# Optimization experiments

Measured on AMD Instinct MI355X. Metric: run time of the kernel, lower is better.

## Reference

```python
import jax, jax.numpy as jnp
import numpy as np

N_HEADS = 16


def _rope(x, cos, sin):
    # x: (B,H,S,hd); cos,sin: (1,1,S,hd//2). Full-dim rotation (rot_dim == head_dim).
    xe = x[..., 0::2]
    xo = x[..., 1::2]
    re = xe * cos - xo * sin
    ro = xe * sin + xo * cos
    return jnp.stack([re, ro], axis=-1).reshape(x.shape)


def setup_inputs() -> dict:
    key = jax.random.key(0)
    B, S, D = 2, 2048, 1024
    hd = D // N_HEADS
    k1, k2, k3, k4, k5 = jax.random.split(key, 5)
    x = jax.random.normal(k1, (B, S, D), dtype=jnp.float32)
    # Linear params (lecun-normal-ish scale)
    w_qkv = jax.random.normal(k2, (D, 3 * D), dtype=jnp.float32) / np.sqrt(D)
    b_qkv = jnp.zeros((3 * D,), dtype=jnp.float32)
    w_out = jax.random.normal(k3, (D, D), dtype=jnp.float32) / np.sqrt(D)
    b_out = jnp.zeros((D,), dtype=jnp.float32)
    # Rotary tables: (S, hd//2)
    inv_freq = 1.0 / (10000.0 ** (np.arange(0, hd, 2, dtype=np.float32) / hd))
    angles = jnp.asarray(np.arange(S, dtype=np.float32)[:, None] * inv_freq[None, :])
    cos = jnp.cos(angles)
    sin = jnp.sin(angles)
    # Causal mask (seq, seq), True = attend
    mask = jnp.tril(jnp.ones((S, S), dtype=bool))
    return {"x": x, "w_qkv": w_qkv, "b_qkv": b_qkv, "w_out": w_out,
            "b_out": b_out, "cos": cos, "sin": sin, "mask": mask}


def reference(x, w_qkv, b_qkv, w_out, b_out, cos, sin, mask):
    B, S, D = x.shape
    H = N_HEADS
    hd = D // H
    scale = hd ** (-0.5)
    qkv = x @ w_qkv + b_qkv  # (B,S,3D)
    qkv = qkv.reshape(B, S, 3, H, hd).transpose(2, 0, 3, 1, 4)  # (3,B,H,S,hd)
    q, k, v = qkv[0], qkv[1], qkv[2]
    c = cos[None, None, :, :]
    s = sin[None, None, :, :]
    q = _rope(q, c, s)
    k = _rope(k, c, s)
    attn = jnp.einsum('bhqd,bhkd->bhqk', q, k) * scale
    attn = jnp.where(mask, attn, -1e9)
    attn = jax.nn.softmax(attn, axis=-1)
    out = jnp.einsum('bhqk,bhkd->bhqd', attn, v)
    out = out.transpose(0, 2, 1, 3).reshape(B, S, D)
    return out @ w_out + b_out
```

## Files before the change

### kernel.cpp

```cpp
#include <hip/hip_runtime.h>
#include <stdint.h>

typedef unsigned short u16;
typedef __attribute__((ext_vector_type(8))) __bf16 bf16x8;
typedef __attribute__((ext_vector_type(4))) float f32x4;
typedef __attribute__((ext_vector_type(4))) unsigned short u16x4;

__device__ __forceinline__ float bf2f(u16 u){
  unsigned int x = ((unsigned int)u) << 16;
  return __builtin_bit_cast(float, x);
}
__device__ __forceinline__ u16 f2bf(float f){
  return __builtin_bit_cast(u16, (__bf16)f);
}
__device__ __forceinline__ float fexp2(float x){ return __builtin_exp2f(x); }
__device__ __forceinline__ void lds_load16(const void* g, void* l){
  __builtin_amdgcn_global_load_lds(
      (const __attribute__((address_space(1))) unsigned int*)g,
      (__attribute__((address_space(3))) unsigned int*)l, 16, 0, 0);
}

__global__ __launch_bounds__(256) void transpose64(const float* __restrict__ in,
                                                   u16* __restrict__ out,
                                                   int R, int C){
  __shared__ u16 t[64][65];
  const int c0 = blockIdx.x * 64, r0 = blockIdx.y * 64;
  const int tid = threadIdx.x;
  const int rr = tid >> 3;
  const int cc = (tid & 7) * 8;
#pragma unroll
  for (int i = 0; i < 2; i++){
    int r = i * 32 + rr;
    const float* p = in + (size_t)(r0 + r) * C + c0 + cc;
    f32x4 v0 = *(const f32x4*)p;
    f32x4 v1 = *(const f32x4*)(p + 4);
#pragma unroll
    for (int j = 0; j < 4; j++){ t[r][cc + j] = f2bf(v0[j]); t[r][cc + 4 + j] = f2bf(v1[j]); }
  }
  __syncthreads();
#pragma unroll
  for (int i = 0; i < 2; i++){
    int c = i * 32 + rr;
    u16 tmp[8];
#pragma unroll
    for (int j = 0; j < 8; j++) tmp[j] = t[cc + j][c];
    *(bf16x8*)(out + (size_t)(c0 + c) * R + r0 + cc) = *(const bf16x8*)tmp;
  }
}

__global__ __launch_bounds__(256) void convert_bf16(const float* __restrict__ in,
                                                    u16* __restrict__ out){
  int t = blockIdx.x * 256 + threadIdx.x;
  const float* p = in + (size_t)t * 8;
  f32x4 v0 = *(const f32x4*)p;
  f32x4 v1 = *(const f32x4*)(p + 4);
  u16 tmp[8];
#pragma unroll
  for (int j = 0; j < 4; j++){ tmp[j] = f2bf(v0[j]); tmp[4 + j] = f2bf(v1[j]); }
  *(bf16x8*)(out + (size_t)t * 8) = *(const bf16x8*)tmp;
}

__global__ __launch_bounds__(256) void v_transpose(const u16* __restrict__ qkv,
                                                   u16* __restrict__ vT){
  const int S = 2048, LD = 3072;
  __shared__ u16 t[64][65];
  const int bh = blockIdx.y;
  const int b = bh >> 4, h = bh & 15;
  const int s0 = blockIdx.x * 64;
  const u16* src = qkv + (size_t)b * S * LD + 2048 + h * 64;
  const int tid = threadIdx.x;
  const int rr = tid >> 3;
  const int cc = (tid & 7) * 8;
#pragma unroll
  for (int i = 0; i < 2; i++){
    int s = i * 32 + rr;
    bf16x8 v = *(const bf16x8*)(src + (size_t)(s0 + s) * LD + cc);
#pragma unroll
    for (int j = 0; j < 8; j++) t[s][cc + j] = __builtin_bit_cast(u16, (__bf16)v[j]);
  }
  __syncthreads();
  u16* dst = vT + (size_t)bh * 64 * S;
#pragma unroll
  for (int i = 0; i < 2; i++){
    int d = i * 32 + rr;
    u16 tmp[8];
#pragma unroll
    for (int j = 0; j < 8; j++) tmp[j] = t[cc + j][d];
    *(bf16x8*)(dst + (size_t)d * S + s0 + cc) = *(const bf16x8*)tmp;
  }
}

template<bool OUTF32, bool ROPE>
__global__ __launch_bounds__(256, 2) void gemm_bt(const u16* __restrict__ A,
                                                  const u16* __restrict__ Bt,
                                                  const float* __restrict__ bias,
                                                  void* __restrict__ Cv,
                                                  int M, int N, int K,
                                                  const float* __restrict__ cosb,
                                                  const float* __restrict__ sinb){
  __shared__ u16 As[128 * 32];
  __shared__ u16 Bs[128 * 32];
  const int nx = gridDim.x;
  const int L = blockIdx.x + nx * blockIdx.y;
  const int per = (nx * gridDim.y) >> 3;
  const int wg = (L & 7) * per + (L >> 3);
  const int bn = wg % nx, bm = wg / nx;
  const int tid = threadIdx.x, w = tid >> 6, l = tid & 63;
  const int lo = l & 15, hi = l >> 4;
  const int wr = (w >> 1) * 64, wc = (w & 1) * 64;
  f32x4 acc[4][4] = {};
  const int lrow = l >> 2, lcd = l & 3;

  for (int k0 = 0; k0 < K; k0 += 32){
#pragma unroll
    for (int i = 0; i < 2; i++){
      int row0 = i * 64 + w * 16;
      int row = row0 + lrow;
      int cs = lcd ^ ((row >> 1) & 3);
      lds_load16(A  + (size_t)(bm * 128 + row) * K + k0 + cs * 8,
                 (char*)As + row0 * 64);
      lds_load16(Bt + (size_t)(bn * 128 + row) * K + k0 + cs * 8,
                 (char*)Bs + row0 * 64);
    }
    __syncthreads();
    bf16x8 a[4], b[4];
#pragma unroll
    for (int mi = 0; mi < 4; mi++){
      int row = wr + mi * 16 + lo;
      unsigned byte = (unsigned)(row * 64 + hi * 16) ^ (((row >> 1) & 3) << 4);
      a[mi] = *(const bf16x8*)((const char*)As + byte);
    }
#pragma unroll
    for (int ni = 0; ni < 4; ni++){
      int row = wc + ni * 16 + lo;
      unsigned byte = (unsigned)(row * 64 + hi * 16) ^ (((row >> 1) & 3) << 4);
      b[ni] = *(const bf16x8*)((const char*)Bs + byte);
    }
    __builtin_amdgcn_s_setprio(1);
#pragma unroll
    for (int mi = 0; mi < 4; mi++)
#pragma unroll
      for (int ni = 0; ni < 4; ni++)
        acc[mi][ni] = __builtin_amdgcn_mfma_f32_16x16x32_bf16(a[mi], b[ni], acc[mi][ni], 0, 0, 0);
    __builtin_amdgcn_s_setprio(0);
    __syncthreads();
  }
  if (ROPE && bn < 16){
#pragma unroll
    for (int mi = 0; mi < 4; mi++){
#pragma unroll
      for (int r = 0; r < 4; r++){
        int grow = bm * 128 + wr + mi * 16 + hi * 4 + r;
        int stok = grow & 2047;
#pragma unroll
        for (int ni = 0; ni < 4; ni++){
          int col = bn * 128 + wc + ni * 16 + lo;
          float v = acc[mi][ni][r] + bias[col];
          float partner = __shfl_xor(v, 1, 64);
          int ip = (col & 63) >> 1;
          float c = cosb[stok * 32 + ip], sn = sinb[stok * 32 + ip];
          float res = (lo & 1) ? (partner * sn + v * c) : (v * c - partner * sn);
          ((u16*)Cv)[(size_t)grow * N + col] = f2bf(res);
        }
      }
    }
  } else {
#pragma unroll
    for (int mi = 0; mi < 4; mi++){
#pragma unroll
      for (int r = 0; r < 4; r++){
        int grow = bm * 128 + wr + mi * 16 + hi * 4 + r;
#pragma unroll
        for (int ni = 0; ni < 4; ni++){
          int col = bn * 128 + wc + ni * 16 + lo;
          float v = acc[mi][ni][r] + bias[col];
          if (OUTF32)
            ((float*)Cv)[(size_t)grow * N + col] = v;
          else
            ((u16*)Cv)[(size_t)grow * N + col] = f2bf(v);
        }
      }
    }
  }
}

__global__ __launch_bounds__(64, 4) void flash_attn(const u16* __restrict__ qkv,
                                                    const u16* __restrict__ vT,
                                                    u16* __restrict__ Oout){
  const int S = 2048, LD = 3072;
  const int L = blockIdx.x;
  const int bh = L & 31;
  const int p = 63 - (L >> 5);
  const int b = bh >> 4, h = bh & 15;
  const u16* base = qkv + (size_t)b * S * LD;
  const u16* Qp = base + h * 64;
  const u16* Kp = base + 1024 + h * 64;
  const u16* Vb = vT + (size_t)bh * 64 * S;
  const int l = threadIdx.x & 63;
  const int lo = l & 15, hi = l >> 4;
  __shared__ u16 Ks[2][32 * 64];
  __shared__ u16 PsA[16 * 36];
  __shared__ u16 PsB[16 * 36];

  const float QSC = 0.125f * 1.44269504089f;
  const int srow8 = l >> 3;
  const int scs = (l & 7) ^ srow8;

  const int q0 = p * 32;
  const int qrowA = q0 + lo;
  const int qrowB = q0 + 16 + lo;
  const int nkt = p + 1;

  bf16x8 qfA0, qfA1, qfB0, qfB1;
  {
    bf16x8 va0 = *(const bf16x8*)(Qp + (size_t)qrowA * LD + hi * 8);
    bf16x8 va1 = *(const bf16x8*)(Qp + (size_t)qrowA * LD + 32 + hi * 8);
    bf16x8 vb0 = *(const bf16x8*)(Qp + (size_t)qrowB * LD + hi * 8);
    bf16x8 vb1 = *(const bf16x8*)(Qp + (size_t)qrowB * LD + 32 + hi * 8);
#pragma unroll
    for (int j = 0; j < 8; j++){
      qfA0[j] = (__bf16)((float)va0[j] * QSC);
      qfA1[j] = (__bf16)((float)va1[j] * QSC);
      qfB0[j] = (__bf16)((float)vb0[j] * QSC);
      qfB1[j] = (__bf16)((float)vb1[j] * QSC);
    }
  }

  f32x4 oA[4] = {}, oB[4] = {};
  float m_rA = -1e30f, l_parA = 0.f;
  float m_rB = -1e30f, l_parB = 0.f;

#pragma unroll
  for (int i = 0; i < 4; i++)
    lds_load16(Kp + (size_t)(i * 8 + srow8) * LD + scs * 8,
               (char*)&Ks[0][0] + i * 1024);

  int cur = 0;
  for (int kt = 0; kt < nkt; kt++){
    bf16x8 vb[4];
#pragma unroll
    for (int fd = 0; fd < 4; fd++)
      vb[fd] = *(const bf16x8*)(Vb + (size_t)(fd * 16 + lo) * S + kt * 32 + hi * 8);
    bf16x8 kb[2][2];
#pragma unroll
    for (int c = 0; c < 2; c++)
#pragma unroll
      for (int f = 0; f < 2; f++){
        int srow = f * 16 + lo;
        unsigned byte = ((unsigned)(srow * 128 + c * 64 + hi * 16)) ^ ((lo & 7) << 4);
        kb[c][f] = *(const bf16x8*)((const char*)&Ks[cur][0] + byte);
      }
    if (kt + 1 < nkt){
#pragma unroll
      for (int i = 0; i < 4; i++)
        lds_load16(Kp + (size_t)((kt + 1) * 32 + i * 8 + srow8) * LD + scs * 8,
                   (char*)&Ks[cur ^ 1][0] + i * 1024);
    }
    f32x4 saA[2] = {}, saB[2] = {};
    __builtin_amdgcn_s_setprio(1);
#pragma unroll
    for (int f = 0; f < 2; f++){
      saA[f] = __builtin_amdgcn_mfma_f32_16x16x32_bf16(kb[0][f], qfA0, saA[f], 0, 0, 0);
      saB[f] = __builtin_amdgcn_mfma_f32_16x16x32_bf16(kb[0][f], qfB0, saB[f], 0, 0, 0);
      saA[f] = __builtin_amdgcn_mfma_f32_16x16x32_bf16(kb[1][f], qfA1, saA[f], 0, 0, 0);
      saB[f] = __builtin_amdgcn_mfma_f32_16x16x32_bf16(kb[1][f], qfB1, saB[f], 0, 0, 0);
    }
    __builtin_amdgcn_s_setprio(0);
    if (kt == nkt - 1){
#pragma unroll
      for (int f = 0; f < 2; f++){
        int key0 = kt * 32 + f * 16 + hi * 4;
#pragma unroll
        for (int r = 0; r < 4; r++){
          if (key0 + r > qrowA) saA[f][r] = -1e30f;
          if (key0 + r > qrowB) saB[f][r] = -1e30f;
        }
      }
    }
    float pmaxA = fmaxf(
        fmaxf(fmaxf(saA[0][0], saA[0][1]), fmaxf(saA[0][2], saA[0][3])),
        fmaxf(fmaxf(saA[1][0], saA[1][1]), fmaxf(saA[1][2], saA[1][3])));
    float pmaxB = fmaxf(
        fmaxf(fmaxf(saB[0][0], saB[0][1]), fmaxf(saB[0][2], saB[0][3])),
        fmaxf(fmaxf(saB[1][0], saB[1][1]), fmaxf(saB[1][2], saB[1][3])));
    if (!__all(fmaxf(pmaxA - m_rA, pmaxB - m_rB) <= 11.5f)){
      float rmA = fmaxf(pmaxA, __shfl_xor(pmaxA, 16, 64));
      rmA = fmaxf(rmA, __shfl_xor(rmA, 32, 64));
      float rmB = fmaxf(pmaxB, __shfl_xor(pmaxB, 16, 64));
      rmB = fmaxf(rmB, __shfl_xor(rmB, 32, 64));
      float mnA = fmaxf(m_rA, rmA), mnB = fmaxf(m_rB, rmB);
      float corrA = fexp2(m_rA - mnA), corrB = fexp2(m_rB - mnB);
      m_rA = mnA; m_rB = mnB;
      l_parA *= corrA; l_parB *= corrB;
      float cqA[4], cqB[4];
#pragma unroll
      for (int r = 0; r < 4; r++){
        cqA[r] = __shfl(corrA, hi * 4 + r, 64);
        cqB[r] = __shfl(corrB, hi * 4 + r, 64);
      }
#pragma unroll
      for (int fd = 0; fd < 4; fd++)
#pragma unroll
        for (int r = 0; r < 4; r++){ oA[fd][r] *= cqA[r]; oB[fd][r] *= cqB[r]; }
    }
    float pvA[2][4], pvB[2][4];
#pragma unroll
    for (int f = 0; f < 2; f++)
#pragma unroll
      for (int r = 0; r < 4; r++){
        pvA[f][r] = fexp2(saA[f][r] - m_rA);
        pvB[f][r] = fexp2(saB[f][r] - m_rB);
      }
#pragma unroll
    for (int f = 0; f < 2; f++){
      u16x4 pkA, pkB;
#pragma unroll
      for (int r = 0; r < 4; r++){ pkA[r] = f2bf(pvA[f][r]); pkB[r] = f2bf(pvB[f][r]); }
      *(u16x4*)((char*)PsA + lo * 72 + f * 32 + hi * 8) = pkA;
      *(u16x4*)((char*)PsB + lo * 72 + f * 32 + hi * 8) = pkB;
    }
    l_parA += ((pvA[0][0] + pvA[0][1]) + (pvA[0][2] + pvA[0][3]))
            + ((pvA[1][0] + pvA[1][1]) + (pvA[1][2] + pvA[1][3]));
    l_parB += ((pvB[0][0] + pvB[0][1]) + (pvB[0][2] + pvB[0][3]))
            + ((pvB[1][0] + pvB[1][1]) + (pvB[1][2] + pvB[1][3]));
    bf16x8 paA = *(const bf16x8*)((const char*)PsA + lo * 72 + hi * 16);
    bf16x8 paB = *(const bf16x8*)((const char*)PsB + lo * 72 + hi * 16);
    __builtin_amdgcn_s_setprio(1);
#pragma unroll
    for (int fd = 0; fd < 4; fd++){
      oA[fd] = __builtin_amdgcn_mfma_f32_16x16x32_bf16(paA, vb[fd], oA[fd], 0, 0, 0);
      oB[fd] = __builtin_amdgcn_mfma_f32_16x16x32_bf16(paB, vb[fd], oB[fd], 0, 0, 0);
    }
    __builtin_amdgcn_s_setprio(0);
    cur ^= 1;
  }
  float lsA = l_parA, lsB = l_parB;
  lsA += __shfl_xor(lsA, 16, 64); lsA += __shfl_xor(lsA, 32, 64);
  lsB += __shfl_xor(lsB, 16, 64); lsB += __shfl_xor(lsB, 32, 64);
  float liA = 1.0f / lsA, liB = 1.0f / lsB;
  float iqA[4], iqB[4];
#pragma unroll
  for (int r = 0; r < 4; r++){
    iqA[r] = __shfl(liA, hi * 4 + r, 64);
    iqB[r] = __shfl(liB, hi * 4 + r, 64);
  }
#pragma unroll
  for (int r = 0; r < 4; r++){
    int srA = q0 + hi * 4 + r;
    int srB = q0 + 16 + hi * 4 + r;
    u16* orA = Oout + (size_t)(b * S + srA) * 1024 + h * 64;
    u16* orB = Oout + (size_t)(b * S + srB) * 1024 + h * 64;
#pragma unroll
    for (int fd = 0; fd < 4; fd++){
      orA[fd * 16 + lo] = f2bf(oA[fd][r] * iqA[r]);
      orB[fd * 16 + lo] = f2bf(oB[fd][r] * iqB[r]);
    }
  }
}

extern "C" void kernel_launch(void* const* d_in, const int* in_sizes, int n_in,
                              void* d_out, int out_size, void* d_ws, size_t ws_size,
                              hipStream_t stream){
  const float* x     = (const float*)d_in[0];
  const float* w_qkv = (const float*)d_in[1];
  const float* b_qkv = (const float*)d_in[2];
  const float* w_out = (const float*)d_in[3];
  const float* b_out = (const float*)d_in[4];
  const float* cosb  = (const float*)d_in[5];
  const float* sinb  = (const float*)d_in[6];
  float* out = (float*)d_out;
  char* ws = (char*)d_ws;
  u16* qkv  = (u16*)(ws);
  u16* attn = (u16*)(ws + 25165824);
  u16* xbf  = attn;
  u16* wT2  = (u16*)(ws + 33554432);
  u16* wT1  = (u16*)(ws + 35651584);
  u16* vT   = (u16*)(ws + 35651584);

  transpose64<<<dim3(48, 16), 256, 0, stream>>>(w_qkv, wT1, 1024, 3072);
  transpose64<<<dim3(16, 16), 256, 0, stream>>>(w_out, wT2, 1024, 1024);
  convert_bf16<<<2048, 256, 0, stream>>>(x, xbf);
  gemm_bt<false, true ><<<dim3(24, 32), 256, 0, stream>>>(xbf, wT1, b_qkv, qkv,
                                                          4096, 3072, 1024, cosb, sinb);
  v_transpose<<<dim3(32, 32), 256, 0, stream>>>(qkv, vT);
  flash_attn<<<2048, 64, 0, stream>>>(qkv, vT, attn);
  gemm_bt<true , false><<<dim3(8, 32), 256, 0, stream>>>(attn, wT2, b_out, out,
                                                         4096, 1024, 1024, cosb, sinb);
}
```

Baseline: 134.4 us.

## Split flash-attention KV range across two waves and deepen GEMM K step

The attention kernel now runs two wavefronts per block. Each wave handles half of the causal key tiles with its own K double buffer, and the two partial softmax states (max, sum, bf16 partial output) are merged through LDS at the end. The GEMM loads two 32-wide K slices per iteration, halving the number of barriers per K. This exposes more parallelism for the long causal rows and amortizes synchronization, at the cost of extra LDS, a bf16-rounded partial output in the merge, and a reused P buffer that serializes the two PV MFMA groups.

Result: no change. 133.4 us (-0.7%).

```diff
diff --git a/kernel.cpp b/kernel.cpp
--- a/kernel.cpp
+++ b/kernel.cpp
@@ -98,8 +98,8 @@
                                                   int M, int N, int K,
                                                   const float* __restrict__ cosb,
                                                   const float* __restrict__ sinb){
-  __shared__ u16 As[128 * 32];
-  __shared__ u16 Bs[128 * 32];
+  __shared__ u16 As[2][128 * 32];
+  __shared__ u16 Bs[2][128 * 32];
   const int nx = gridDim.x;
   const int L = blockIdx.x + nx * blockIdx.y;
   const int per = (nx * gridDim.y) >> 3;
@@ -111,38 +111,44 @@
   f32x4 acc[4][4] = {};
   const int lrow = l >> 2, lcd = l & 3;
 
-  for (int k0 = 0; k0 < K; k0 += 32){
-#pragma unroll
-    for (int i = 0; i < 2; i++){
-      int row0 = i * 64 + w * 16;
-      int row = row0 + lrow;
-      int cs = lcd ^ ((row >> 1) & 3);
-      lds_load16(A  + (size_t)(bm * 128 + row) * K + k0 + cs * 8,
-                 (char*)As + row0 * 64);
-      lds_load16(Bt + (size_t)(bn * 128 + row) * K + k0 + cs * 8,
-                 (char*)Bs + row0 * 64);
+  for (int k0 = 0; k0 < K; k0 += 64){
+#pragma unroll
+    for (int p = 0; p < 2; p++){
+#pragma unroll
+      for (int i = 0; i < 2; i++){
+        int row0 = i * 64 + w * 16;
+        int row = row0 + lrow;
+        int cs = lcd ^ ((row >> 1) & 3);
+        lds_load16(A  + (size_t)(bm * 128 + row) * K + k0 + p * 32 + cs * 8,
+                   (char*)&As[p][0] + row0 * 64);
+        lds_load16(Bt + (size_t)(bn * 128 + row) * K + k0 + p * 32 + cs * 8,
+                   (char*)&Bs[p][0] + row0 * 64);
+      }
     }
     __syncthreads();
-    bf16x8 a[4], b[4];
-#pragma unroll
-    for (int mi = 0; mi < 4; mi++){
-      int row = wr + mi * 16 + lo;
-      unsigned byte = (unsigned)(row * 64 + hi * 16) ^ (((row >> 1) & 3) << 4);
-      a[mi] = *(const bf16x8*)((const char*)As + byte);
-    }
-#pragma unroll
-    for (int ni = 0; ni < 4; ni++){
-      int row = wc + ni * 16 + lo;
-      unsigned byte = (unsigned)(row * 64 + hi * 16) ^ (((row >> 1) & 3) << 4);
-      b[ni] = *(const bf16x8*)((const char*)Bs + byte);
-    }
-    __builtin_amdgcn_s_setprio(1);
-#pragma unroll
-    for (int mi = 0; mi < 4; mi++)
-#pragma unroll
-      for (int ni = 0; ni < 4; ni++)
-        acc[mi][ni] = __builtin_amdgcn_mfma_f32_16x16x32_bf16(a[mi], b[ni], acc[mi][ni], 0, 0, 0);
-    __builtin_amdgcn_s_setprio(0);
+#pragma unroll
+    for (int p = 0; p < 2; p++){
+      bf16x8 a[4], b[4];
+#pragma unroll
+      for (int mi = 0; mi < 4; mi++){
+        int row = wr + mi * 16 + lo;
+        unsigned byte = (unsigned)(row * 64 + hi * 16) ^ (((row >> 1) & 3) << 4);
+        a[mi] = *(const bf16x8*)((const char*)&As[p][0] + byte);
+      }
+#pragma unroll
+      for (int ni = 0; ni < 4; ni++){
+        int row = wc + ni * 16 + lo;
+        unsigned byte = (unsigned)(row * 64 + hi * 16) ^ (((row >> 1) & 3) << 4);
+        b[ni] = *(const bf16x8*)((const char*)&Bs[p][0] + byte);
+      }
+      __builtin_amdgcn_s_setprio(1);
+#pragma unroll
+      for (int mi = 0; mi < 4; mi++)
+#pragma unroll
+        for (int ni = 0; ni < 4; ni++)
+          acc[mi][ni] = __builtin_amdgcn_mfma_f32_16x16x32_bf16(a[mi], b[ni], acc[mi][ni], 0, 0, 0);
+      __builtin_amdgcn_s_setprio(0);
+    }
     __syncthreads();
   }
   if (ROPE && bn < 16){
@@ -184,39 +190,42 @@
   }
 }
 
-__global__ __launch_bounds__(64, 4) void flash_attn(const u16* __restrict__ qkv,
-                                                    const u16* __restrict__ vT,
-                                                    u16* __restrict__ Oout){
+__global__ __launch_bounds__(128, 2) void flash_attn(const u16* __restrict__ qkv,
+                                                     const u16* __restrict__ vT,
+                                                     u16* __restrict__ Oout){
   const int S = 2048, LD = 3072;
   const int L = blockIdx.x;
   const int bh = L & 31;
-  const int p = 63 - (L >> 5);
+  const int T = 63 - (L >> 5);
   const int b = bh >> 4, h = bh & 15;
   const u16* base = qkv + (size_t)b * S * LD;
   const u16* Qp = base + h * 64;
   const u16* Kp = base + 1024 + h * 64;
   const u16* Vb = vT + (size_t)bh * 64 * S;
-  const int l = threadIdx.x & 63;
+  const int tid = threadIdx.x, w = tid >> 6, l = tid & 63;
   const int lo = l & 15, hi = l >> 4;
-  __shared__ u16 Ks[2][32 * 64];
-  __shared__ u16 PsA[16 * 36];
-  __shared__ u16 PsB[16 * 36];
+  __shared__ u16 Ks[2][2][32 * 64];
+  __shared__ u16 arena[2304];
+  __shared__ float Xm[32], Xl[32];
 
   const float QSC = 0.125f * 1.44269504089f;
   const int srow8 = l >> 3;
   const int scs = (l & 7) ^ srow8;
 
-  const int q0 = p * 32;
-  const int qrowA = q0 + lo;
-  const int qrowB = q0 + 16 + lo;
-  const int nkt = p + 1;
+  const int q0 = T * 32;
+  const int qrA = q0 + lo, qrB = q0 + 16 + lo;
+  const int nkt = T + 1;
+  const int ch = (nkt + 1) >> 1;
+  const int k0 = w ? ch : 0;
+  const int k1 = w ? nkt : ch;
+  u16* Ps = arena + w * 576;
 
   bf16x8 qfA0, qfA1, qfB0, qfB1;
   {
-    bf16x8 va0 = *(const bf16x8*)(Qp + (size_t)qrowA * LD + hi * 8);
-    bf16x8 va1 = *(const bf16x8*)(Qp + (size_t)qrowA * LD + 32 + hi * 8);
-    bf16x8 vb0 = *(const bf16x8*)(Qp + (size_t)qrowB * LD + hi * 8);
-    bf16x8 vb1 = *(const bf16x8*)(Qp + (size_t)qrowB * LD + 32 + hi * 8);
+    bf16x8 va0 = *(const bf16x8*)(Qp + (size_t)qrA * LD + hi * 8);
+    bf16x8 va1 = *(const bf16x8*)(Qp + (size_t)qrA * LD + 32 + hi * 8);
+    bf16x8 vb0 = *(const bf16x8*)(Qp + (size_t)qrB * LD + hi * 8);
+    bf16x8 vb1 = *(const bf16x8*)(Qp + (size_t)qrB * LD + 32 + hi * 8);
 #pragma unroll
     for (int j = 0; j < 8; j++){
       qfA0[j] = (__bf16)((float)va0[j] * QSC);
@@ -227,16 +236,17 @@
   }
 
   f32x4 oA[4] = {}, oB[4] = {};
-  float m_rA = -1e30f, l_parA = 0.f;
-  float m_rB = -1e30f, l_parB = 0.f;
-
-#pragma unroll
-  for (int i = 0; i < 4; i++)
-    lds_load16(Kp + (size_t)(i * 8 + srow8) * LD + scs * 8,
-               (char*)&Ks[0][0] + i * 1024);
-
+  float mA = -1e30f, mB = -1e30f;
+  float lparA = 0.f, lparB = 0.f;
+
+  if (k0 < k1){
+#pragma unroll
+    for (int i = 0; i < 4; i++)
+      lds_load16(Kp + (size_t)(k0 * 32 + i * 8 + srow8) * LD + scs * 8,
+                 (char*)&Ks[w][0][0] + i * 1024);
+  }
   int cur = 0;
-  for (int kt = 0; kt < nkt; kt++){
+  for (int kt = k0; kt < k1; kt++){
     bf16x8 vb[4];
 #pragma unroll
     for (int fd = 0; fd < 4; fd++)
@@ -246,15 +256,15 @@
     for (int c = 0; c < 2; c++)
 #pragma unroll
       for (int f = 0; f < 2; f++){
-        int srow = f * 16 + lo;
-        unsigned byte = ((unsigned)(srow * 128 + c * 64 + hi * 16)) ^ ((lo & 7) << 4);
-        kb[c][f] = *(const bf16x8*)((const char*)&Ks[cur][0] + byte);
-      }
-    if (kt + 1 < nkt){
+        int srw = f * 16 + lo;
+        unsigned byte = ((unsigned)(srw * 128 + c * 64 + hi * 16)) ^ ((lo & 7) << 4);
+        kb[c][f] = *(const bf16x8*)((const char*)&Ks[w][cur][0] + byte);
+      }
+    if (kt + 1 < k1){
 #pragma unroll
       for (int i = 0; i < 4; i++)
         lds_load16(Kp + (size_t)((kt + 1) * 32 + i * 8 + srow8) * LD + scs * 8,
-                   (char*)&Ks[cur ^ 1][0] + i * 1024);
+                   (char*)&Ks[w][cur ^ 1][0] + i * 1024);
     }
     f32x4 saA[2] = {}, saB[2] = {};
     __builtin_amdgcn_s_setprio(1);
@@ -272,31 +282,31 @@
         int key0 = kt * 32 + f * 16 + hi * 4;
 #pragma unroll
         for (int r = 0; r < 4; r++){
-          if (key0 + r > qrowA) saA[f][r] = -1e30f;
-          if (key0 + r > qrowB) saB[f][r] = -1e30f;
+          if (key0 + r > qrA) saA[f][r] = -1e30f;
+          if (key0 + r > qrB) saB[f][r] = -1e30f;
         }
       }
     }
-    float pmaxA = fmaxf(
+    float pmA = fmaxf(
         fmaxf(fmaxf(saA[0][0], saA[0][1]), fmaxf(saA[0][2], saA[0][3])),
         fmaxf(fmaxf(saA[1][0], saA[1][1]), fmaxf(saA[1][2], saA[1][3])));
-    float pmaxB = fmaxf(
+    float pmB = fmaxf(
         fmaxf(fmaxf(saB[0][0], saB[0][1]), fmaxf(saB[0][2], saB[0][3])),
         fmaxf(fmaxf(saB[1][0], saB[1][1]), fmaxf(saB[1][2], saB[1][3])));
-    if (!__all(fmaxf(pmaxA - m_rA, pmaxB - m_rB) <= 11.5f)){
-      float rmA = fmaxf(pmaxA, __shfl_xor(pmaxA, 16, 64));
+    if (!__all(fmaxf(pmA - mA, pmB - mB) <= 11.5f)){
+      float rmA = fmaxf(pmA, __shfl_xor(pmA, 16, 64));
       rmA = fmaxf(rmA, __shfl_xor(rmA, 32, 64));
-      float rmB = fmaxf(pmaxB, __shfl_xor(pmaxB, 16, 64));
+      float rmB = fmaxf(pmB, __shfl_xor(pmB, 16, 64));
       rmB = fmaxf(rmB, __shfl_xor(rmB, 32, 64));
-      float mnA = fmaxf(m_rA, rmA), mnB = fmaxf(m_rB, rmB);
-      float corrA = fexp2(m_rA - mnA), corrB = fexp2(m_rB - mnB);
-      m_rA = mnA; m_rB = mnB;
-      l_parA *= corrA; l_parB *= corrB;
+      float mnA = fmaxf(mA, rmA), mnB = fmaxf(mB, rmB);
+      float cA = fexp2(mA - mnA), cB = fexp2(mB - mnB);
+      mA = mnA; mB = mnB;
+      lparA *= cA; lparB *= cB;
       float cqA[4], cqB[4];
 #pragma unroll
       for (int r = 0; r < 4; r++){
-        cqA[r] = __shfl(corrA, hi * 4 + r, 64);
-        cqB[r] = __shfl(corrB, hi * 4 + r, 64);
+        cqA[r] = __shfl(cA, hi * 4 + r, 64);
+        cqB[r] = __shfl(cB, hi * 4 + r, 64);
       }
 #pragma unroll
       for (int fd = 0; fd < 4; fd++)
@@ -308,52 +318,91 @@
     for (int f = 0; f < 2; f++)
 #pragma unroll
       for (int r = 0; r < 4; r++){
-        pvA[f][r] = fexp2(saA[f][r] - m_rA);
-        pvB[f][r] = fexp2(saB[f][r] - m_rB);
-      }
+        pvA[f][r] = fexp2(saA[f][r] - mA);
+        pvB[f][r] = fexp2(saB[f][r] - mB);
+      }
+    lparA += ((pvA[0][0] + pvA[0][1]) + (pvA[0][2] + pvA[0][3]))
+           + ((pvA[1][0] + pvA[1][1]) + (pvA[1][2] + pvA[1][3]));
+    lparB += ((pvB[0][0] + pvB[0][1]) + (pvB[0][2] + pvB[0][3]))
+           + ((pvB[1][0] + pvB[1][1]) + (pvB[1][2] + pvB[1][3]));
 #pragma unroll
     for (int f = 0; f < 2; f++){
-      u16x4 pkA, pkB;
-#pragma unroll
-      for (int r = 0; r < 4; r++){ pkA[r] = f2bf(pvA[f][r]); pkB[r] = f2bf(pvB[f][r]); }
-      *(u16x4*)((char*)PsA + lo * 72 + f * 32 + hi * 8) = pkA;
-      *(u16x4*)((char*)PsB + lo * 72 + f * 32 + hi * 8) = pkB;
-    }
-    l_parA += ((pvA[0][0] + pvA[0][1]) + (pvA[0][2] + pvA[0][3]))
-            + ((pvA[1][0] + pvA[1][1]) + (pvA[1][2] + pvA[1][3]));
-    l_parB += ((pvB[0][0] + pvB[0][1]) + (pvB[0][2] + pvB[0][3]))
-            + ((pvB[1][0] + pvB[1][1]) + (pvB[1][2] + pvB[1][3]));
-    bf16x8 paA = *(const bf16x8*)((const char*)PsA + lo * 72 + hi * 16);
-    bf16x8 paB = *(const bf16x8*)((const char*)PsB + lo * 72 + hi * 16);
+      u16x4 pk;
+#pragma unroll
+      for (int r = 0; r < 4; r++) pk[r] = f2bf(pvA[f][r]);
+      *(u16x4*)((char*)Ps + lo * 72 + f * 32 + hi * 8) = pk;
+    }
+    bf16x8 paA = *(const bf16x8*)((const char*)Ps + lo * 72 + hi * 16);
     __builtin_amdgcn_s_setprio(1);
 #pragma unroll
-    for (int fd = 0; fd < 4; fd++){
+    for (int fd = 0; fd < 4; fd++)
       oA[fd] = __builtin_amdgcn_mfma_f32_16x16x32_bf16(paA, vb[fd], oA[fd], 0, 0, 0);
+    __builtin_amdgcn_s_setprio(0);
+#pragma unroll
+    for (int f = 0; f < 2; f++){
+      u16x4 pk;
+#pragma unroll
+      for (int r = 0; r < 4; r++) pk[r] = f2bf(pvB[f][r]);
+      *(u16x4*)((char*)Ps + lo * 72 + f * 32 + hi * 8) = pk;
+    }
+    bf16x8 paB = *(const bf16x8*)((const char*)Ps + lo * 72 + hi * 16);
+    __builtin_amdgcn_s_setprio(1);
+#pragma unroll
+    for (int fd = 0; fd < 4; fd++)
       oB[fd] = __builtin_amdgcn_mfma_f32_16x16x32_bf16(paB, vb[fd], oB[fd], 0, 0, 0);
-    }
     __builtin_amdgcn_s_setprio(0);
     cur ^= 1;
   }
-  float lsA = l_parA, lsB = l_parB;
-  lsA += __shfl_xor(lsA, 16, 64); lsA += __shfl_xor(lsA, 32, 64);
-  lsB += __shfl_xor(lsB, 16, 64); lsB += __shfl_xor(lsB, 32, 64);
-  float liA = 1.0f / lsA, liB = 1.0f / lsB;
-  float iqA[4], iqB[4];
-#pragma unroll
-  for (int r = 0; r < 4; r++){
-    iqA[r] = __shfl(liA, hi * 4 + r, 64);
-    iqB[r] = __shfl(liB, hi * 4 + r, 64);
-  }
-#pragma unroll
-  for (int r = 0; r < 4; r++){
-    int srA = q0 + hi * 4 + r;
-    int srB = q0 + 16 + hi * 4 + r;
-    u16* orA = Oout + (size_t)(b * S + srA) * 1024 + h * 64;
-    u16* orB = Oout + (size_t)(b * S + srB) * 1024 + h * 64;
+  lparA += __shfl_xor(lparA, 16, 64); lparA += __shfl_xor(lparA, 32, 64);
+  lparB += __shfl_xor(lparB, 16, 64); lparB += __shfl_xor(lparB, 32, 64);
+
+  __syncthreads();
+  if (w == 1){
 #pragma unroll
     for (int fd = 0; fd < 4; fd++){
-      orA[fd * 16 + lo] = f2bf(oA[fd][r] * iqA[r]);
-      orB[fd * 16 + lo] = f2bf(oB[fd][r] * iqB[r]);
+      u16x4 pkA, pkB;
+#pragma unroll
+      for (int r = 0; r < 4; r++){ pkA[r] = f2bf(oA[fd][r]); pkB[r] = f2bf(oB[fd][r]); }
+      *(u16x4*)((char*)arena + (fd * 16 + lo) * 72 + hi * 8) = pkA;
+      *(u16x4*)((char*)arena + (fd * 16 + lo) * 72 + 32 + hi * 8) = pkB;
+    }
+    if (hi == 0){
+      Xm[lo] = mA;      Xl[lo] = lparA;
+      Xm[16 + lo] = mB; Xl[16 + lo] = lparB;
+    }
+  }
+  __syncthreads();
+  if (w == 0){
+    u16x4 pA[4], pB[4];
+#pragma unroll
+    for (int fd = 0; fd < 4; fd++){
+      pA[fd] = *(const u16x4*)((const char*)arena + (fd * 16 + lo) * 72 + hi * 8);
+      pB[fd] = *(const u16x4*)((const char*)arena + (fd * 16 + lo) * 72 + 32 + hi * 8);
+    }
+#pragma unroll
+    for (int r = 0; r < 4; r++){
+      float mOA = __shfl(mA, hi * 4 + r, 64);
+      float lOA = __shfl(lparA, hi * 4 + r, 64);
+      float mOB = __shfl(mB, hi * 4 + r, 64);
+      float lOB = __shfl(lparB, hi * 4 + r, 64);
+      float mPA = Xm[hi * 4 + r], lPA = Xl[hi * 4 + r];
+      float mPB = Xm[16 + hi * 4 + r], lPB = Xl[16 + hi * 4 + r];
+      float MfA = fmaxf(mOA, mPA), MfB = fmaxf(mOB, mPB);
+      float c0A = fexp2(mOA - MfA), c1A = fexp2(mPA - MfA);
+      float c0B = fexp2(mOB - MfB), c1B = fexp2(mPB - MfB);
+      float invA = 1.0f / (lOA * c0A + lPA * c1A);
+      float invB = 1.0f / (lOB * c0B + lPB * c1B);
+      int srA = q0 + hi * 4 + r;
+      int srB = q0 + 16 + hi * 4 + r;
+      u16* orA = Oout + (size_t)(b * S + srA) * 1024 + h * 64;
+      u16* orB = Oout + (size_t)(b * S + srB) * 1024 + h * 64;
+#pragma unroll
+      for (int fd = 0; fd < 4; fd++){
+        float vA = (oA[fd][r] * c0A + bf2f(pA[fd][r]) * c1A) * invA;
+        float vB = (oB[fd][r] * c0B + bf2f(pB[fd][r]) * c1B) * invB;
+        orA[fd * 16 + lo] = f2bf(vA);
+        orB[fd * 16 + lo] = f2bf(vB);
+      }
     }
   }
 }
@@ -383,7 +432,7 @@
   gemm_bt<false, true ><<<dim3(24, 32), 256, 0, stream>>>(xbf, wT1, b_qkv, qkv,
                                                           4096, 3072, 1024, cosb, sinb);
   v_transpose<<<dim3(32, 32), 256, 0, stream>>>(qkv, vT);
-  flash_attn<<<2048, 64, 0, stream>>>(qkv, vT, attn);
+  flash_attn<<<2048, 128, 0, stream>>>(qkv, vT, attn);
   gemm_bt<true , false><<<dim3(8, 32), 256, 0, stream>>>(attn, wT2, b_out, out,
                                                          4096, 1024, 1024, cosb, sinb);
 }
```
